# Performance work log

Hardware: AMD Instinct MI355X
Metric: run time of the kernel (lower is better)

The kernel has to match this reference:

```python
import jax, jax.numpy as jnp
import numpy as np

B, T, C, H, E, K = 4, 2048, 1024, 2048, 8, 2


def setup_inputs() -> dict:
    key = jax.random.key(0)
    ks = jax.random.split(key, 9)
    s = lambda k, shape, fan: jax.random.normal(k, shape, jnp.float32) / np.sqrt(fan)
    return {
        "x": jax.random.normal(ks[0], (B, T, C), jnp.float32),
        "gate_w": s(ks[1], (C, E), C),            # router gate (no bias)
        "sg_w": s(ks[2], (C, H), C),              # shared expert: gate proj
        "su_w": s(ks[3], (C, H), C),              # shared expert: up proj
        "sd_w": s(ks[4], (H, C), H),              # shared expert: down proj
        "eg_w": s(ks[5], (E, C, H), C),           # routed experts: gate proj
        "eu_w": s(ks[6], (E, C, H), C),           # routed experts: up proj
        "ed_w": s(ks[7], (E, H, C), H),           # routed experts: down proj
    }


def _swiglu(x, wg, wu, wd):
    # x: (B,T,C) -> (B,T,C)
    return jnp.einsum("bth,hc->btc", jax.nn.silu(jnp.einsum("btc,ch->bth", x, wg)) * jnp.einsum("btc,ch->bth", x, wu), wd)


def reference(x, gate_w, sg_w, su_w, sd_w, eg_w, eu_w, ed_w):
    # Router: top-k over expert logits, softmax over selected logits
    logits = jnp.einsum("btc,ce->bte", x, gate_w)            # (B,T,E)
    topk_logits, topk_idx = jax.lax.top_k(logits, K)         # (B,T,K)
    weights = jax.nn.softmax(topk_logits, axis=-1)           # (B,T,K)
    # Dense per-expert combine weight: w_e[b,t,e] = sum_k weights*(idx==e)
    onehot = jax.nn.one_hot(topk_idx, E, dtype=x.dtype)      # (B,T,K,E)
    dense_w = jnp.einsum("btk,btke->bte", weights, onehot)   # (B,T,E)

    shared_out = _swiglu(x, sg_w, su_w, sd_w)

    # Scan over experts (small fixed E), accumulating weighted expert outputs.
    dense_w_e = jnp.moveaxis(dense_w, -1, 0)                 # (E,B,T)

    def step(acc, params):
        wg, wu, wd, w = params
        return acc + w[..., None] * _swiglu(x, wg, wu, wd), None

    expert_out, _ = jax.lax.scan(step, jnp.zeros_like(x), (eg_w, eu_w, ed_w, dense_w_e))
    return shared_out + expert_out, logits
```

## Files before the change

### kernel.cpp

```cpp
#include <hip/hip_runtime.h>
#include <cstdint>
#include <cstddef>

#define NTOK 8192
#define CDIM 1024
#define HDIM 2048
#define NEXP 8
#define NSEG 9
#define MAXTILES 104

typedef __bf16 bf16;
typedef unsigned short u16;
typedef __attribute__((ext_vector_type(8))) __bf16 bf16x8;
typedef __attribute__((ext_vector_type(4))) float f32x4;

__device__ __forceinline__ u16 f2bf(float f) {
  union { u16 u; __bf16 b; } cv;
  cv.b = (__bf16)f;
  return cv.u;
}

__device__ __forceinline__ void gload_lds16(const bf16* g, bf16* l) {
  __builtin_amdgcn_global_load_lds(
      (const __attribute__((address_space(1))) unsigned int*)g,
      (__attribute__((address_space(3))) unsigned int*)l, 16, 0, 0);
}

__global__ __launch_bounds__(64) void init_kernel(int* __restrict__ counts,
                                                  int* __restrict__ fill) {
  if (threadIdx.x < NEXP) {
    counts[threadIdx.x] = 0;
    fill[threadIdx.x] = 0;
  }
}

__global__ __launch_bounds__(256) void zero_out_kernel(float* __restrict__ out) {
  size_t i = ((size_t)blockIdx.x * 256 + threadIdx.x) * 8;
  float4 z = {0.f, 0.f, 0.f, 0.f};
  *(float4*)(out + i) = z;
  *(float4*)(out + i + 4) = z;
}

__global__ __launch_bounds__(256) void cast_x_kernel(
    const float* __restrict__ src, bf16* __restrict__ dst) {
  size_t i = ((size_t)blockIdx.x * 256 + threadIdx.x) * 8;
  float4 a = *(const float4*)(src + i);
  float4 b = *(const float4*)(src + i + 4);
  bf16x8 p;
  p[0] = (bf16)a.x; p[1] = (bf16)a.y; p[2] = (bf16)a.z; p[3] = (bf16)a.w;
  p[4] = (bf16)b.x; p[5] = (bf16)b.y; p[6] = (bf16)b.z; p[7] = (bf16)b.w;
  *(bf16x8*)(dst + i) = p;
}

__global__ __launch_bounds__(256) void router2_kernel(
    const float* __restrict__ x, const float* __restrict__ gw,
    float* __restrict__ logits_out, int* __restrict__ tk_e,
    float* __restrict__ tk_w, int* __restrict__ counts) {
  int wv = threadIdx.x >> 6, l = threadIdx.x & 63;
  int t = blockIdx.x * 4 + wv;
  const float* xr = x + (size_t)t * CDIM;
  float acc[NEXP];
#pragma unroll
  for (int e = 0; e < NEXP; ++e) acc[e] = 0.f;
  for (int c = l; c < CDIM; c += 64) {
    float xv = xr[c];
    const float* g = gw + (size_t)c * NEXP;
    float4 g0 = *(const float4*)(g);
    float4 g1 = *(const float4*)(g + 4);
    acc[0] += xv * g0.x; acc[1] += xv * g0.y; acc[2] += xv * g0.z; acc[3] += xv * g0.w;
    acc[4] += xv * g1.x; acc[5] += xv * g1.y; acc[6] += xv * g1.z; acc[7] += xv * g1.w;
  }
#pragma unroll
  for (int off = 32; off > 0; off >>= 1) {
#pragma unroll
    for (int e = 0; e < NEXP; ++e) acc[e] += __shfl_xor(acc[e], off, 64);
  }
  int e0 = 0; float l0 = acc[0];
#pragma unroll
  for (int e = 1; e < NEXP; ++e) { if (acc[e] > l0) { l0 = acc[e]; e0 = e; } }
  int e1 = -1; float l1 = -3.4e38f;
#pragma unroll
  for (int e = 0; e < NEXP; ++e) { if (e != e0 && acc[e] > l1) { l1 = acc[e]; e1 = e; } }
  float ex = expf(l1 - l0);
  float w0 = 1.f / (1.f + ex), w1 = ex / (1.f + ex);
  if (l < NEXP) logits_out[(size_t)t * NEXP + l] = acc[l];
  if (l == 0) {
    tk_e[2 * t] = e0; tk_e[2 * t + 1] = e1;
    tk_w[2 * t] = w0; tk_w[2 * t + 1] = w1;
    atomicAdd(&counts[e0], 1);
    atomicAdd(&counts[e1], 1);
  }
}

__global__ __launch_bounds__(256) void offsets_kernel(
    const int* __restrict__ counts, int* __restrict__ offs_g,
    int* __restrict__ tile_seg, int* __restrict__ list_tok,
    float* __restrict__ w_row) {
  __shared__ int off[NSEG], pad[NSEG], cnt[NSEG], ntot;
  int tid = threadIdx.x;
  if (tid == 0) {
    int tot = 0;
    for (int e = 0; e < NSEG; ++e) {
      int c = (e < NEXP) ? counts[e] : NTOK;
      cnt[e] = c; off[e] = tot;
      int p = (c + 255) & ~255;
      pad[e] = p; tot += p;
    }
    ntot = tot;
  }
  __syncthreads();
  if (tid < NSEG) offs_g[tid] = off[tid];
  for (int gt = tid; gt < MAXTILES; gt += 256) {
    int row = gt * 256, seg = -1;
    if (row < ntot) {
      for (int e = 0; e < NSEG; ++e)
        if (row >= off[e] && row < off[e] + pad[e]) { seg = e; break; }
    }
    tile_seg[gt] = seg;
  }
  for (int e = 0; e < NSEG; ++e)
    for (int i = off[e] + cnt[e] + tid; i < off[e] + pad[e]; i += 256) {
      list_tok[i] = 0;
      w_row[i] = 0.f;
    }
}

__global__ __launch_bounds__(256) void scatter_kernel(
    const int* __restrict__ tk_e, const float* __restrict__ tk_w,
    const int* __restrict__ offs, int* __restrict__ fill,
    int* __restrict__ list_tok, float* __restrict__ w_row) {
  int t = blockIdx.x * 256 + threadIdx.x;
  int e0 = tk_e[2 * t], e1 = tk_e[2 * t + 1];
  float w0 = tk_w[2 * t], w1 = tk_w[2 * t + 1];
  int p0 = atomicAdd(&fill[e0], 1);
  int i0 = offs[e0] + p0;
  list_tok[i0] = t; w_row[i0] = w0;
  int p1 = atomicAdd(&fill[e1], 1);
  int i1 = offs[e1] + p1;
  list_tok[i1] = t; w_row[i1] = w1;
  int rsh = offs[NEXP] + t;
  list_tok[rsh] = t; w_row[rsh] = 1.f;
}

__device__ __forceinline__ void transpose_body(const float* __restrict__ src,
                                               u16* __restrict__ dst, int R, int C) {
  __shared__ u16 tile[64][65];
  int r0 = blockIdx.y * 64, c0 = blockIdx.x * 64;
  int tr = threadIdx.x >> 2;
  int tc = (threadIdx.x & 3) * 16;
  const float* s = src + (size_t)(r0 + tr) * C + c0 + tc;
  float4 f[4];
#pragma unroll
  for (int q = 0; q < 4; ++q) f[q] = *(const float4*)(s + q * 4);
#pragma unroll
  for (int q = 0; q < 4; ++q) {
    tile[tr][tc + q * 4 + 0] = f2bf(f[q].x);
    tile[tr][tc + q * 4 + 1] = f2bf(f[q].y);
    tile[tr][tc + q * 4 + 2] = f2bf(f[q].z);
    tile[tr][tc + q * 4 + 3] = f2bf(f[q].w);
  }
  __syncthreads();
  union { uint4 v[2]; u16 e[16]; } u;
#pragma unroll
  for (int j = 0; j < 16; ++j) u.e[j] = tile[tc + j][tr];
  u16* d = dst + (size_t)(c0 + tr) * R + r0 + tc;
  *(uint4*)d = u.v[0];
  *(uint4*)(d + 8) = u.v[1];
}

__global__ __launch_bounds__(256) void transpose_cast_kernel(
    const float* __restrict__ src, u16* __restrict__ dst, int R, int C) {
  transpose_body(src, dst, R, C);
}

__global__ __launch_bounds__(256) void transpose_gu_kernel(
    const float* __restrict__ sg, const float* __restrict__ su,
    const float* __restrict__ eg, const float* __restrict__ eu,
    u16* __restrict__ wTg, u16* __restrict__ wTu) {
  const size_t slot = (size_t)HDIM * CDIM;
  int z = blockIdx.z;
  const float* src; u16* dst;
  if (z == 0)       { src = sg;                 dst = wTg + 8 * slot; }
  else if (z == 1)  { src = su;                 dst = wTu + 8 * slot; }
  else if (z < 10)  { src = eg + (z - 2) * slot;  dst = wTg + (z - 2) * slot; }
  else              { src = eu + (z - 10) * slot; dst = wTu + (z - 10) * slot; }
  transpose_body(src, dst, CDIM, HDIM);
}

__global__ __launch_bounds__(256) void transpose_d_kernel(
    const float* __restrict__ sd, const float* __restrict__ ed,
    u16* __restrict__ wTd) {
  const size_t slot = (size_t)HDIM * CDIM;
  int z = blockIdx.z;
  const float* src; u16* dst;
  if (z == 0) { src = sd;                 dst = wTd + 8 * slot; }
  else        { src = ed + (z - 1) * slot; dst = wTd + (z - 1) * slot; }
  transpose_body(src, dst, HDIM, CDIM);
}


__global__ __launch_bounds__(512, 2) void gemm_gu4(
    const bf16* __restrict__ xb, const bf16* __restrict__ wTg,
    const bf16* __restrict__ wTu, const int* __restrict__ tile_seg,
    const int* __restrict__ list_tok, bf16* __restrict__ act) {
  __shared__ __align__(16) bf16 sS[2][32768];
  __shared__ int tokLds[256];

  const int nwg = gridDim.x;
  const int bid = blockIdx.x;
  const int wid = (bid & 7) * (nwg >> 3) + (bid >> 3);
  const int tileIdx = wid % MAXTILES;
  const int colIdx = wid / MAXTILES;
  const int seg = tile_seg[tileIdx];
  if (seg < 0) return;

  const int tid = threadIdx.x, l = tid & 63, wv = tid >> 6;
  const int wr = wv >> 2, wn = wv & 3;
  const int n0 = colIdx * 128;
  const size_t rowbase = (size_t)tileIdx * 256;

  if (tid < 256) tokLds[tid] = list_tok[rowbase + tid];
  __syncthreads();

  const int row8 = tid >> 3;
  const int scol = (((tid & 7) ^ (row8 & 7)) << 3);
  const bf16* gA0 = xb + (size_t)tokLds[row8] * CDIM + scol;
  const bf16* gA1 = xb + (size_t)tokLds[128 + row8] * CDIM + scol;
  const bf16* gA2 = xb + (size_t)tokLds[64 + row8] * CDIM + scol;
  const bf16* gA3 = xb + (size_t)tokLds[192 + row8] * CDIM + scol;
  const size_t wslot = (size_t)seg * HDIM * CDIM;
  const bf16* gBg = wTg + wslot + (size_t)(n0 + row8) * CDIM + scol;
  const bf16* gBu = wTu + wslot + (size_t)(n0 + row8) * CDIM + scol;
  const int t8 = tid * 8;

  const int fr = l & 15, kq = l >> 4;
  const int cS0 = ((kq ^ (l & 7)) << 4);
  const int cS1 = (((4 | kq) ^ (l & 7)) << 4);
  const int aBase = (wr * 128 + fr) * 128;
  const int gBase = 32768 + (wn * 32 + fr) * 128;
  const int uBase = 49152 + (wn * 32 + fr) * 128;

  f32x4 accG[2][4][2], accU[2][4][2];
#pragma unroll
  for (int h = 0; h < 2; ++h)
#pragma unroll
    for (int i = 0; i < 4; ++i)
#pragma unroll
      for (int j = 0; j < 2; ++j) {
        accG[h][i][j] = (f32x4){0.f, 0.f, 0.f, 0.f};
        accU[h][i][j] = (f32x4){0.f, 0.f, 0.f, 0.f};
      }

  auto stC0 = [&](int b, int k0) { bf16* d = &sS[b][0];
    gload_lds16(gBg + k0, d + 16384 + t8);
    gload_lds16(gBg + 64 * CDIM + k0, d + 20480 + t8); };
  auto stC1 = [&](int b, int k0) { bf16* d = &sS[b][0];
    gload_lds16(gA0 + k0, d + t8);
    gload_lds16(gA1 + k0, d + 8192 + t8); };
  auto stC2 = [&](int b, int k0) { bf16* d = &sS[b][0];
    gload_lds16(gBu + k0, d + 24576 + t8);
    gload_lds16(gBu + 64 * CDIM + k0, d + 28672 + t8); };
  auto stC3 = [&](int b, int k0) { bf16* d = &sS[b][0];
    gload_lds16(gA2 + k0, d + 4096 + t8);
    gload_lds16(gA3 + k0, d + 12288 + t8); };

  constexpr int NKT = CDIM / 64;
  stC0(0, 0); stC1(0, 0); stC2(0, 0); stC3(0, 0);

  for (int kt = 0; kt < NKT; ++kt) {
    const int b = kt & 1, bn = b ^ 1;
    const int kn = (kt + 1) * 64;
    const bool more = (kt + 1 < NKT);
    const char* pS = (const char*)&sS[b][0];
    bf16x8 af[4][2], bg[2][2], bu[2][2];

    asm volatile("s_waitcnt vmcnt(4)" ::: "memory");
    __builtin_amdgcn_s_barrier();
#pragma unroll
    for (int i = 0; i < 4; ++i) {
      af[i][0] = *(const bf16x8*)(pS + aBase + i * 2048 + cS0);
      af[i][1] = *(const bf16x8*)(pS + aBase + i * 2048 + cS1);
    }
#pragma unroll
    for (int j = 0; j < 2; ++j) {
      bg[j][0] = *(const bf16x8*)(pS + gBase + j * 2048 + cS0);
      bg[j][1] = *(const bf16x8*)(pS + gBase + j * 2048 + cS1);
    }
    if (more) stC0(bn, kn);
    asm volatile("s_waitcnt lgkmcnt(0)" ::: "memory");
    __builtin_amdgcn_sched_barrier(0);
    __builtin_amdgcn_s_setprio(1);
#pragma unroll
    for (int i = 0; i < 4; ++i)
#pragma unroll
      for (int j = 0; j < 2; ++j) {
        accG[0][i][j] = __builtin_amdgcn_mfma_f32_16x16x32_bf16(af[i][0], bg[j][0], accG[0][i][j], 0, 0, 0);
        accG[0][i][j] = __builtin_amdgcn_mfma_f32_16x16x32_bf16(af[i][1], bg[j][1], accG[0][i][j], 0, 0, 0);
      }
    __builtin_amdgcn_s_setprio(0);

    if (more) asm volatile("s_waitcnt vmcnt(4)" ::: "memory");
    else      asm volatile("s_waitcnt vmcnt(2)" ::: "memory");
    __builtin_amdgcn_s_barrier();
#pragma unroll
    for (int j = 0; j < 2; ++j) {
      bu[j][0] = *(const bf16x8*)(pS + uBase + j * 2048 + cS0);
      bu[j][1] = *(const bf16x8*)(pS + uBase + j * 2048 + cS1);
    }
    if (more) stC1(bn, kn);
    asm volatile("s_waitcnt lgkmcnt(0)" ::: "memory");
    __builtin_amdgcn_sched_barrier(0);
    __builtin_amdgcn_s_setprio(1);
#pragma unroll
    for (int i = 0; i < 4; ++i)
#pragma unroll
      for (int j = 0; j < 2; ++j) {
        accU[0][i][j] = __builtin_amdgcn_mfma_f32_16x16x32_bf16(af[i][0], bu[j][0], accU[0][i][j], 0, 0, 0);
        accU[0][i][j] = __builtin_amdgcn_mfma_f32_16x16x32_bf16(af[i][1], bu[j][1], accU[0][i][j], 0, 0, 0);
      }
    __builtin_amdgcn_s_setprio(0);

    if (more) asm volatile("s_waitcnt vmcnt(4)" ::: "memory");
    else      asm volatile("s_waitcnt vmcnt(0)" ::: "memory");
    __builtin_amdgcn_s_barrier();
#pragma unroll
    for (int i = 0; i < 4; ++i) {
      af[i][0] = *(const bf16x8*)(pS + aBase + 8192 + i * 2048 + cS0);
      af[i][1] = *(const bf16x8*)(pS + aBase + 8192 + i * 2048 + cS1);
    }
    if (more) stC2(bn, kn);
    asm volatile("s_waitcnt lgkmcnt(0)" ::: "memory");
    __builtin_amdgcn_sched_barrier(0);
    __builtin_amdgcn_s_setprio(1);
#pragma unroll
    for (int i = 0; i < 4; ++i)
#pragma unroll
      for (int j = 0; j < 2; ++j) {
        accG[1][i][j] = __builtin_amdgcn_mfma_f32_16x16x32_bf16(af[i][0], bg[j][0], accG[1][i][j], 0, 0, 0);
        accG[1][i][j] = __builtin_amdgcn_mfma_f32_16x16x32_bf16(af[i][1], bg[j][1], accG[1][i][j], 0, 0, 0);
      }
    __builtin_amdgcn_s_setprio(0);

    __builtin_amdgcn_s_barrier();
    if (more) stC3(bn, kn);
    __builtin_amdgcn_s_setprio(1);
#pragma unroll
    for (int i = 0; i < 4; ++i)
#pragma unroll
      for (int j = 0; j < 2; ++j) {
        accU[1][i][j] = __builtin_amdgcn_mfma_f32_16x16x32_bf16(af[i][0], bu[j][0], accU[1][i][j], 0, 0, 0);
        accU[1][i][j] = __builtin_amdgcn_mfma_f32_16x16x32_bf16(af[i][1], bu[j][1], accU[1][i][j], 0, 0, 0);
      }
    __builtin_amdgcn_s_setprio(0);
  }

  const int cn = n0 + wn * 32 + fr;
  const int rb = wr * 128 + kq * 4;
#pragma unroll
  for (int h = 0; h < 2; ++h)
#pragma unroll
    for (int i = 0; i < 4; ++i)
#pragma unroll
      for (int r = 0; r < 4; ++r) {
        const size_t row = rowbase + rb + h * 64 + i * 16 + r;
#pragma unroll
        for (int j = 0; j < 2; ++j) {
          float g = accG[h][i][j][r], uu = accU[h][i][j][r];
          float s = g / (1.f + expf(-g));
          act[row * HDIM + cn + j * 16] = (bf16)(s * uu);
        }
      }
}

__global__ __launch_bounds__(512, 2) void gemm_down4(
    const bf16* __restrict__ act, const bf16* __restrict__ wTd,
    const int* __restrict__ tile_seg, const int* __restrict__ list_tok,
    const float* __restrict__ w_row, float* __restrict__ out) {
  __shared__ __align__(16) bf16 sS[2][24576];
  __shared__ int tokLds[256];
  __shared__ float wLds[256];

  const int nwg = gridDim.x;
  const int bid = blockIdx.x;
  const int wid = (bid & 7) * (nwg >> 3) + (bid >> 3);
  const int tileIdx = wid % MAXTILES;
  const int colIdx = wid / MAXTILES;
  const int seg = tile_seg[tileIdx];
  if (seg < 0) return;

  const int tid = threadIdx.x, l = tid & 63, wv = tid >> 6;
  const int wr = wv >> 2, wn = wv & 3;
  const int n0 = colIdx * 128;
  const size_t rowbase = (size_t)tileIdx * 256;

  if (tid < 256) tokLds[tid] = list_tok[rowbase + tid];
  else           wLds[tid - 256] = w_row[rowbase + tid - 256];
  __syncthreads();

  const int row8 = tid >> 3;
  const int scol = (((tid & 7) ^ (row8 & 7)) << 3);
  const bf16* gA0 = act + (rowbase + row8) * HDIM + scol;
  const bf16* gA1 = act + (rowbase + 128 + row8) * HDIM + scol;
  const bf16* gA2 = act + (rowbase + 64 + row8) * HDIM + scol;
  const bf16* gA3 = act + (rowbase + 192 + row8) * HDIM + scol;
  const bf16* gB  = wTd + (size_t)seg * CDIM * HDIM + (size_t)(n0 + row8) * HDIM + scol;
  const int t8 = tid * 8;

  const int fr = l & 15, kq = l >> 4;
  const int cS0 = ((kq ^ (l & 7)) << 4);
  const int cS1 = (((4 | kq) ^ (l & 7)) << 4);
  const int aBase = (wr * 128 + fr) * 128;
  const int bBase = 32768 + (wn * 32 + fr) * 128;

  f32x4 acc[2][4][2];
#pragma unroll
  for (int h = 0; h < 2; ++h)
#pragma unroll
    for (int i = 0; i < 4; ++i)
#pragma unroll
      for (int j = 0; j < 2; ++j) acc[h][i][j] = (f32x4){0.f, 0.f, 0.f, 0.f};

  auto stC0 = [&](int b, int k0) { bf16* d = &sS[b][0];
    gload_lds16(gB + k0, d + 16384 + t8);
    gload_lds16(gB + 64 * HDIM + k0, d + 20480 + t8); };
  auto stC1 = [&](int b, int k0) { bf16* d = &sS[b][0];
    gload_lds16(gA0 + k0, d + t8);
    gload_lds16(gA1 + k0, d + 8192 + t8); };
  auto stC2 = [&](int b, int k0) { bf16* d = &sS[b][0];
    gload_lds16(gA2 + k0, d + 4096 + t8);
    gload_lds16(gA3 + k0, d + 12288 + t8); };

  constexpr int NKT = HDIM / 64;
  stC0(0, 0); stC1(0, 0); stC2(0, 0);

  for (int kt = 0; kt < NKT; ++kt) {
    const int b = kt & 1, bn = b ^ 1;
    const int kn = (kt + 1) * 64;
    const bool more = (kt + 1 < NKT);
    const char* pS = (const char*)&sS[b][0];
    bf16x8 af[4][2], bf[2][2];

    asm volatile("s_waitcnt vmcnt(2)" ::: "memory");
    __builtin_amdgcn_s_barrier();
#pragma unroll
    for (int i = 0; i < 4; ++i) {
      af[i][0] = *(const bf16x8*)(pS + aBase + i * 2048 + cS0);
      af[i][1] = *(const bf16x8*)(pS + aBase + i * 2048 + cS1);
    }
#pragma unroll
    for (int j = 0; j < 2; ++j) {
      bf[j][0] = *(const bf16x8*)(pS + bBase + j * 2048 + cS0);
      bf[j][1] = *(const bf16x8*)(pS + bBase + j * 2048 + cS1);
    }
    if (more) { stC0(bn, kn); stC1(bn, kn); }
    asm volatile("s_waitcnt lgkmcnt(0)" ::: "memory");
    __builtin_amdgcn_sched_barrier(0);
    __builtin_amdgcn_s_setprio(1);
#pragma unroll
    for (int i = 0; i < 4; ++i)
#pragma unroll
      for (int j = 0; j < 2; ++j) {
        acc[0][i][j] = __builtin_amdgcn_mfma_f32_16x16x32_bf16(af[i][0], bf[j][0], acc[0][i][j], 0, 0, 0);
        acc[0][i][j] = __builtin_amdgcn_mfma_f32_16x16x32_bf16(af[i][1], bf[j][1], acc[0][i][j], 0, 0, 0);
      }
    __builtin_amdgcn_s_setprio(0);

    if (more) asm volatile("s_waitcnt vmcnt(4)" ::: "memory");
    else      asm volatile("s_waitcnt vmcnt(0)" ::: "memory");
    __builtin_amdgcn_s_barrier();
#pragma unroll
    for (int i = 0; i < 4; ++i) {
      af[i][0] = *(const bf16x8*)(pS + aBase + 8192 + i * 2048 + cS0);
      af[i][1] = *(const bf16x8*)(pS + aBase + 8192 + i * 2048 + cS1);
    }
    if (more) stC2(bn, kn);
    asm volatile("s_waitcnt lgkmcnt(0)" ::: "memory");
    __builtin_amdgcn_sched_barrier(0);
    __builtin_amdgcn_s_setprio(1);
#pragma unroll
    for (int i = 0; i < 4; ++i)
#pragma unroll
      for (int j = 0; j < 2; ++j) {
        acc[1][i][j] = __builtin_amdgcn_mfma_f32_16x16x32_bf16(af[i][0], bf[j][0], acc[1][i][j], 0, 0, 0);
        acc[1][i][j] = __builtin_amdgcn_mfma_f32_16x16x32_bf16(af[i][1], bf[j][1], acc[1][i][j], 0, 0, 0);
      }
    __builtin_amdgcn_s_setprio(0);
  }

  const int cn = n0 + wn * 32 + fr;
  const int rb = wr * 128 + kq * 4;
#pragma unroll
  for (int h = 0; h < 2; ++h)
#pragma unroll
    for (int i = 0; i < 4; ++i)
#pragma unroll
      for (int r = 0; r < 4; ++r) {
        const int lrow = rb + h * 64 + i * 16 + r;
        const float w = wLds[lrow];
        if (w != 0.f) {
          const int tok = tokLds[lrow];
          float* op = out + (size_t)tok * CDIM + cn;
#pragma unroll
          for (int j = 0; j < 2; ++j)
            atomicAdd(op + j * 16, w * acc[h][i][j][r]);
        }
      }
}

__global__ __launch_bounds__(256) void router_kernel(
    const float* __restrict__ x, const float* __restrict__ gw,
    float* __restrict__ dense_w, float* __restrict__ logits_out) {
  int wv = threadIdx.x >> 6, l = threadIdx.x & 63;
  int t = blockIdx.x * 4 + wv;
  const float* xr = x + (size_t)t * CDIM;
  float acc[NEXP];
#pragma unroll
  for (int e = 0; e < NEXP; ++e) acc[e] = 0.f;
  for (int c = l; c < CDIM; c += 64) {
    float xv = xr[c];
    const float* g = gw + (size_t)c * NEXP;
    float4 g0 = *(const float4*)(g);
    float4 g1 = *(const float4*)(g + 4);
    acc[0] += xv * g0.x; acc[1] += xv * g0.y; acc[2] += xv * g0.z; acc[3] += xv * g0.w;
    acc[4] += xv * g1.x; acc[5] += xv * g1.y; acc[6] += xv * g1.z; acc[7] += xv * g1.w;
  }
#pragma unroll
  for (int off = 32; off > 0; off >>= 1) {
#pragma unroll
    for (int e = 0; e < NEXP; ++e) acc[e] += __shfl_xor(acc[e], off, 64);
  }
  int e0 = 0; float l0 = acc[0];
#pragma unroll
  for (int e = 1; e < NEXP; ++e) { if (acc[e] > l0) { l0 = acc[e]; e0 = e; } }
  int e1 = -1; float l1 = -3.4e38f;
#pragma unroll
  for (int e = 0; e < NEXP; ++e) { if (e != e0 && acc[e] > l1) { l1 = acc[e]; e1 = e; } }
  float ex = expf(l1 - l0);
  float w0 = 1.f / (1.f + ex), w1 = ex / (1.f + ex);
  if (l < NEXP) {
    dense_w[(size_t)t * NEXP + l] = (l == e0) ? w0 : ((l == e1) ? w1 : 0.f);
    logits_out[(size_t)t * NEXP + l] = acc[l];
  }
}

template <int MODE>
__global__ __launch_bounds__(256) void gemm_bt(
    const bf16* __restrict__ A, const bf16* __restrict__ Bt,
    int K, int N,
    bf16* __restrict__ Dbf, const bf16* __restrict__ Gin,
    float* __restrict__ outAcc, const float* __restrict__ denseW, int expertId) {
  __shared__ __align__(16) bf16 sA[128 * 32];
  __shared__ __align__(16) bf16 sB[128 * 32];
  const int tid = threadIdx.x;
  const int l = tid & 63, wv = tid >> 6;
  const int wr = wv >> 1, wc = wv & 1;
  const int m0 = blockIdx.y * 128, n0 = blockIdx.x * 128;
  f32x4 acc[4][4];
#pragma unroll
  for (int i = 0; i < 4; ++i)
#pragma unroll
    for (int j = 0; j < 4; ++j) acc[i][j] = (f32x4){0.f, 0.f, 0.f, 0.f};
  const int srow = wv * 16 + (l >> 2);
  const int scol = (l & 3) * 8;
  const bf16* gA = A + (size_t)(m0 + srow) * K + scol;
  const bf16* gB = Bt + (size_t)(n0 + srow) * K + scol;
  bf16* lA = sA + srow * 32 + scol;
  bf16* lB = sB + srow * 32 + scol;
  const int fr = l & 15, fk = (l >> 4) * 8;
  const bf16* rA = sA + (size_t)(wr * 64 + fr) * 32 + fk;
  const bf16* rB = sB + (size_t)(wc * 64 + fr) * 32 + fk;
  for (int k0 = 0; k0 < K; k0 += 32) {
    __syncthreads();
    gload_lds16(gA, lA);
    gload_lds16(gA + (size_t)64 * K, lA + 64 * 32);
    gload_lds16(gB, lB);
    gload_lds16(gB + (size_t)64 * K, lB + 64 * 32);
    gA += 32; gB += 32;
    __syncthreads();
    bf16x8 af[4], bfr[4];
#pragma unroll
    for (int i = 0; i < 4; ++i) af[i] = *(const bf16x8*)(rA + i * 16 * 32);
#pragma unroll
    for (int j = 0; j < 4; ++j) bfr[j] = *(const bf16x8*)(rB + j * 16 * 32);
#pragma unroll
    for (int i = 0; i < 4; ++i)
#pragma unroll
      for (int j = 0; j < 4; ++j)
        acc[i][j] = __builtin_amdgcn_mfma_f32_16x16x32_bf16(af[i], bfr[j], acc[i][j], 0, 0, 0);
  }
  const int cn = n0 + wc * 64 + (l & 15);
  const int rb = m0 + wr * 64 + (l >> 4) * 4;
#pragma unroll
  for (int i = 0; i < 4; ++i)
#pragma unroll
    for (int r = 0; r < 4; ++r) {
      const int m = rb + i * 16 + r;
#pragma unroll
      for (int j = 0; j < 4; ++j) {
        const int n = cn + j * 16;
        float v = acc[i][j][r];
        if (MODE == 0) {
          Dbf[(size_t)m * N + n] = (bf16)v;
        } else if (MODE == 1) {
          float g = (float)Gin[(size_t)m * N + n];
          float s = g / (1.f + expf(-g));
          Dbf[(size_t)m * N + n] = (bf16)(s * v);
        } else if (MODE == 2) {
          outAcc[(size_t)m * N + n] = v;
        } else {
          float w = denseW[(size_t)m * NEXP + expertId];
          outAcc[(size_t)m * N + n] += w * v;
        }
      }
    }
}

extern "C" void kernel_launch(void* const* d_in, const int* in_sizes, int n_in,
                              void* d_out, int out_size, void* d_ws, size_t ws_size,
                              hipStream_t stream) {
  const float* x    = (const float*)d_in[0];
  const float* gate = (const float*)d_in[1];
  const float* sg   = (const float*)d_in[2];
  const float* su   = (const float*)d_in[3];
  const float* sd   = (const float*)d_in[4];
  const float* eg   = (const float*)d_in[5];
  const float* eu   = (const float*)d_in[6];
  const float* ed   = (const float*)d_in[7];
  float* out    = (float*)d_out;
  float* logits = out + (size_t)NTOK * CDIM;

  const size_t MB = 1u << 20;
  const size_t full_need = 226 * MB;

  if (ws_size >= full_need) {
    char* ws = (char*)d_ws;
    bf16*  xb   = (bf16*)(ws);
    bf16*  wTg  = (bf16*)(ws + 16 * MB);
    bf16*  wTu  = (bf16*)(ws + 52 * MB);
    bf16*  act  = (bf16*)(ws + 88 * MB);
    bf16*  wTd  = (bf16*)(ws + 16 * MB);
    char*  sm   = ws + 224 * MB;
    int*   list_tok = (int*)(sm);
    int*   tk_e     = (int*)(sm + 256 * 1024);
    float* tk_w     = (float*)(sm + 320 * 1024);
    int*   tile_seg = (int*)(sm + 384 * 1024);
    int*   counts   = (int*)(sm + 388 * 1024);
    int*   fill     = (int*)(sm + 389 * 1024);
    int*   offs     = (int*)(sm + 390 * 1024);
    float* w_row    = (float*)(sm + 400 * 1024);

    init_kernel<<<1, 64, 0, stream>>>(counts, fill);
    zero_out_kernel<<<NTOK * CDIM / (256 * 8), 256, 0, stream>>>(out);
    cast_x_kernel<<<NTOK * CDIM / (256 * 8), 256, 0, stream>>>(x, xb);
    router2_kernel<<<NTOK / 4, 256, 0, stream>>>(x, gate, logits, tk_e, tk_w, counts);
    offsets_kernel<<<1, 256, 0, stream>>>(counts, offs, tile_seg, list_tok, w_row);
    scatter_kernel<<<NTOK / 256, 256, 0, stream>>>(tk_e, tk_w, offs, fill, list_tok, w_row);

    dim3 tgu(HDIM / 64, CDIM / 64, 18);
    transpose_gu_kernel<<<tgu, 256, 0, stream>>>(sg, su, eg, eu, (u16*)wTg, (u16*)wTu);

    gemm_gu4<<<(HDIM / 128) * MAXTILES, 512, 0, stream>>>(xb, wTg, wTu, tile_seg, list_tok, act);

    dim3 tdd(CDIM / 64, HDIM / 64, 9);
    transpose_d_kernel<<<tdd, 256, 0, stream>>>(sd, ed, (u16*)wTd);

    gemm_down4<<<(CDIM / 128) * MAXTILES, 512, 0, stream>>>(act, wTd, tile_seg, list_tok, w_row, out);
    return;
  }

  char* ws = (char*)d_ws;
  bf16*  xb   = (bf16*)(ws);
  bf16*  wTgf = (bf16*)(ws + 16 * MB);
  bf16*  wTuf = (bf16*)(ws + 20 * MB);
  bf16*  wTdf = (bf16*)(ws + 24 * MB);
  bf16*  gbuf = (bf16*)(ws + 28 * MB);
  float* dw   = (float*)(ws + 60 * MB);
  if (ws_size < 60 * MB + (size_t)NTOK * NEXP * sizeof(float)) return;

  cast_x_kernel<<<NTOK * CDIM / (256 * 8), 256, 0, stream>>>(x, xb);
  router_kernel<<<NTOK / 4, 256, 0, stream>>>(x, gate, dw, logits);

  dim3 tg1(HDIM / 64, CDIM / 64);
  dim3 tg2(CDIM / 64, HDIM / 64);
  dim3 g1(HDIM / 128, NTOK / 128);
  dim3 g2(CDIM / 128, NTOK / 128);

  transpose_cast_kernel<<<tg1, 256, 0, stream>>>(sg, (u16*)wTgf, CDIM, HDIM);
  transpose_cast_kernel<<<tg1, 256, 0, stream>>>(su, (u16*)wTuf, CDIM, HDIM);
  transpose_cast_kernel<<<tg2, 256, 0, stream>>>(sd, (u16*)wTdf, HDIM, CDIM);
  gemm_bt<0><<<g1, 256, 0, stream>>>(xb, wTgf, CDIM, HDIM, gbuf, nullptr, nullptr, nullptr, 0);
  gemm_bt<1><<<g1, 256, 0, stream>>>(xb, wTuf, CDIM, HDIM, gbuf, gbuf, nullptr, nullptr, 0);
  gemm_bt<2><<<g2, 256, 0, stream>>>(gbuf, wTdf, HDIM, CDIM, nullptr, nullptr, out, nullptr, 0);

  for (int e = 0; e < NEXP; ++e) {
    const float* egp = eg + (size_t)e * CDIM * HDIM;
    const float* eup = eu + (size_t)e * CDIM * HDIM;
    const float* edp = ed + (size_t)e * HDIM * CDIM;
    transpose_cast_kernel<<<tg1, 256, 0, stream>>>(egp, (u16*)wTgf, CDIM, HDIM);
    transpose_cast_kernel<<<tg1, 256, 0, stream>>>(eup, (u16*)wTuf, CDIM, HDIM);
    transpose_cast_kernel<<<tg2, 256, 0, stream>>>(edp, (u16*)wTdf, HDIM, CDIM);
    gemm_bt<0><<<g1, 256, 0, stream>>>(xb, wTgf, CDIM, HDIM, gbuf, nullptr, nullptr, nullptr, 0);
    gemm_bt<1><<<g1, 256, 0, stream>>>(xb, wTuf, CDIM, HDIM, gbuf, gbuf, nullptr, nullptr, 0);
    gemm_bt<3><<<g2, 256, 0, stream>>>(gbuf, wTdf, HDIM, CDIM, nullptr, nullptr, out, dw, e);
  }
}
```

Baseline: 969.1 us.

## Replace atomic scatter-add in down GEMM with bf16 buffer plus gather combine

The down-projection GEMM now writes its per-row results as bf16 into a dense buffer instead of doing weighted float atomicAdds into the output. A new combine kernel uses an inverse index map to gather each token's shared and two expert rows, weight them and write the output once, which also removes the output zeroing kernel and the w_row array. The transpose-cast body is also rewritten to pack two bf16 rows into 32-bit LDS words for wider shared-memory access. The trade is an extra kernel and buffer round trip, plus bf16 rounding of the intermediate expert outputs.

```diff
diff --git a/kernel.cpp b/kernel.cpp
--- a/kernel.cpp
+++ b/kernel.cpp
@@ -32,13 +32,6 @@
     counts[threadIdx.x] = 0;
     fill[threadIdx.x] = 0;
   }
-}
-
-__global__ __launch_bounds__(256) void zero_out_kernel(float* __restrict__ out) {
-  size_t i = ((size_t)blockIdx.x * 256 + threadIdx.x) * 8;
-  float4 z = {0.f, 0.f, 0.f, 0.f};
-  *(float4*)(out + i) = z;
-  *(float4*)(out + i + 4) = z;
 }
 
 __global__ __launch_bounds__(256) void cast_x_kernel(
@@ -94,8 +87,7 @@
 
 __global__ __launch_bounds__(256) void offsets_kernel(
     const int* __restrict__ counts, int* __restrict__ offs_g,
-    int* __restrict__ tile_seg, int* __restrict__ list_tok,
-    float* __restrict__ w_row) {
+    int* __restrict__ tile_seg, int* __restrict__ list_tok) {
   __shared__ int off[NSEG], pad[NSEG], cnt[NSEG], ntot;
   int tid = threadIdx.x;
   if (tid == 0) {
@@ -119,51 +111,56 @@
     tile_seg[gt] = seg;
   }
   for (int e = 0; e < NSEG; ++e)
-    for (int i = off[e] + cnt[e] + tid; i < off[e] + pad[e]; i += 256) {
+    for (int i = off[e] + cnt[e] + tid; i < off[e] + pad[e]; i += 256)
       list_tok[i] = 0;
-      w_row[i] = 0.f;
-    }
 }
 
 __global__ __launch_bounds__(256) void scatter_kernel(
-    const int* __restrict__ tk_e, const float* __restrict__ tk_w,
-    const int* __restrict__ offs, int* __restrict__ fill,
-    int* __restrict__ list_tok, float* __restrict__ w_row) {
+    const int* __restrict__ tk_e, const int* __restrict__ offs,
+    int* __restrict__ fill, int* __restrict__ list_tok,
+    int* __restrict__ inv) {
   int t = blockIdx.x * 256 + threadIdx.x;
   int e0 = tk_e[2 * t], e1 = tk_e[2 * t + 1];
-  float w0 = tk_w[2 * t], w1 = tk_w[2 * t + 1];
   int p0 = atomicAdd(&fill[e0], 1);
   int i0 = offs[e0] + p0;
-  list_tok[i0] = t; w_row[i0] = w0;
+  list_tok[i0] = t; inv[2 * t] = i0;
   int p1 = atomicAdd(&fill[e1], 1);
   int i1 = offs[e1] + p1;
-  list_tok[i1] = t; w_row[i1] = w1;
-  int rsh = offs[NEXP] + t;
-  list_tok[rsh] = t; w_row[rsh] = 1.f;
+  list_tok[i1] = t; inv[2 * t + 1] = i1;
+  list_tok[offs[NEXP] + t] = t;
 }
 
 __device__ __forceinline__ void transpose_body(const float* __restrict__ src,
                                                u16* __restrict__ dst, int R, int C) {
-  __shared__ u16 tile[64][65];
-  int r0 = blockIdx.y * 64, c0 = blockIdx.x * 64;
-  int tr = threadIdx.x >> 2;
-  int tc = (threadIdx.x & 3) * 16;
-  const float* s = src + (size_t)(r0 + tr) * C + c0 + tc;
-  float4 f[4];
-#pragma unroll
-  for (int q = 0; q < 4; ++q) f[q] = *(const float4*)(s + q * 4);
-#pragma unroll
-  for (int q = 0; q < 4; ++q) {
-    tile[tr][tc + q * 4 + 0] = f2bf(f[q].x);
-    tile[tr][tc + q * 4 + 1] = f2bf(f[q].y);
-    tile[tr][tc + q * 4 + 2] = f2bf(f[q].z);
-    tile[tr][tc + q * 4 + 3] = f2bf(f[q].w);
-  }
+  __shared__ uint32_t t32[64 * 33];
+  const int tid = threadIdx.x;
+  const int r0 = blockIdx.y * 64, c0 = blockIdx.x * 64;
+  const int rp = tid >> 3;
+  const int cg = tid & 7;
+  const float* s0 = src + (size_t)(r0 + 2 * rp) * C + c0 + 8 * cg;
+  const float* s1 = s0 + C;
+  float4 a0 = *(const float4*)(s0);
+  float4 a1 = *(const float4*)(s0 + 4);
+  float4 b0 = *(const float4*)(s1);
+  float4 b1 = *(const float4*)(s1 + 4);
+  uint32_t p[8];
+  p[0] = f2bf(a0.x) | ((uint32_t)f2bf(b0.x) << 16);
+  p[1] = f2bf(a0.y) | ((uint32_t)f2bf(b0.y) << 16);
+  p[2] = f2bf(a0.z) | ((uint32_t)f2bf(b0.z) << 16);
+  p[3] = f2bf(a0.w) | ((uint32_t)f2bf(b0.w) << 16);
+  p[4] = f2bf(a1.x) | ((uint32_t)f2bf(b1.x) << 16);
+  p[5] = f2bf(a1.y) | ((uint32_t)f2bf(b1.y) << 16);
+  p[6] = f2bf(a1.z) | ((uint32_t)f2bf(b1.z) << 16);
+  p[7] = f2bf(a1.w) | ((uint32_t)f2bf(b1.w) << 16);
+#pragma unroll
+  for (int c = 0; c < 8; ++c) t32[(8 * cg + c) * 33 + rp] = p[c];
   __syncthreads();
-  union { uint4 v[2]; u16 e[16]; } u;
-#pragma unroll
-  for (int j = 0; j < 16; ++j) u.e[j] = tile[tc + j][tr];
-  u16* d = dst + (size_t)(c0 + tr) * R + r0 + tc;
+  const int oc = tid >> 2, og = tid & 3;
+  const uint32_t* rb = &t32[oc * 33 + 8 * og];
+  union { uint32_t w[8]; uint4 v[2]; } u;
+#pragma unroll
+  for (int k = 0; k < 8; ++k) u.w[k] = rb[k];
+  u16* d = dst + (size_t)(c0 + oc) * R + r0 + 16 * og;
   *(uint4*)d = u.v[0];
   *(uint4*)(d + 8) = u.v[1];
 }
@@ -374,11 +371,8 @@
 
 __global__ __launch_bounds__(512, 2) void gemm_down4(
     const bf16* __restrict__ act, const bf16* __restrict__ wTd,
-    const int* __restrict__ tile_seg, const int* __restrict__ list_tok,
-    const float* __restrict__ w_row, float* __restrict__ out) {
+    const int* __restrict__ tile_seg, bf16* __restrict__ dbuf) {
   __shared__ __align__(16) bf16 sS[2][24576];
-  __shared__ int tokLds[256];
-  __shared__ float wLds[256];
 
   const int nwg = gridDim.x;
   const int bid = blockIdx.x;
@@ -392,10 +386,6 @@
   const int wr = wv >> 2, wn = wv & 3;
   const int n0 = colIdx * 128;
   const size_t rowbase = (size_t)tileIdx * 256;
-
-  if (tid < 256) tokLds[tid] = list_tok[rowbase + tid];
-  else           wLds[tid - 256] = w_row[rowbase + tid - 256];
-  __syncthreads();
 
   const int row8 = tid >> 3;
   const int scol = (((tid & 7) ^ (row8 & 7)) << 3);
@@ -495,16 +485,29 @@
     for (int i = 0; i < 4; ++i)
 #pragma unroll
       for (int r = 0; r < 4; ++r) {
-        const int lrow = rb + h * 64 + i * 16 + r;
-        const float w = wLds[lrow];
-        if (w != 0.f) {
-          const int tok = tokLds[lrow];
-          float* op = out + (size_t)tok * CDIM + cn;
-#pragma unroll
-          for (int j = 0; j < 2; ++j)
-            atomicAdd(op + j * 16, w * acc[h][i][j][r]);
-        }
-      }
+        const size_t row = rowbase + rb + h * 64 + i * 16 + r;
+#pragma unroll
+        for (int j = 0; j < 2; ++j)
+          dbuf[row * CDIM + cn + j * 16] = (bf16)acc[h][i][j][r];
+      }
+}
+
+__global__ __launch_bounds__(128) void combine_kernel(
+    const bf16* __restrict__ dbuf, const int* __restrict__ offs,
+    const int* __restrict__ inv, const float* __restrict__ tk_w,
+    float* __restrict__ out) {
+  const int t = blockIdx.x;
+  const int c = threadIdx.x * 8;
+  const int rsh = offs[NEXP] + t;
+  const int i0 = inv[2 * t], i1 = inv[2 * t + 1];
+  const float w0 = tk_w[2 * t], w1 = tk_w[2 * t + 1];
+  bf16x8 a = *(const bf16x8*)(dbuf + (size_t)rsh * CDIM + c);
+  bf16x8 b = *(const bf16x8*)(dbuf + (size_t)i0 * CDIM + c);
+  bf16x8 d = *(const bf16x8*)(dbuf + (size_t)i1 * CDIM + c);
+  float* op = out + (size_t)t * CDIM + c;
+#pragma unroll
+  for (int j = 0; j < 8; ++j)
+    op[j] = (float)a[j] + w0 * (float)b[j] + w1 * (float)d[j];
 }
 
 __global__ __launch_bounds__(256) void router_kernel(
@@ -638,23 +641,23 @@
     bf16*  wTg  = (bf16*)(ws + 16 * MB);
     bf16*  wTu  = (bf16*)(ws + 52 * MB);
     bf16*  act  = (bf16*)(ws + 88 * MB);
-    bf16*  wTd  = (bf16*)(ws + 16 * MB);
-    char*  sm   = ws + 224 * MB;
+    bf16*  wTd  = (bf16*)(ws);
+    bf16*  dbuf = (bf16*)(ws + 36 * MB);
+    char*  sm   = ws + 200 * MB;
     int*   list_tok = (int*)(sm);
+    int*   inv      = (int*)(sm + 128 * 1024);
     int*   tk_e     = (int*)(sm + 256 * 1024);
     float* tk_w     = (float*)(sm + 320 * 1024);
     int*   tile_seg = (int*)(sm + 384 * 1024);
     int*   counts   = (int*)(sm + 388 * 1024);
     int*   fill     = (int*)(sm + 389 * 1024);
     int*   offs     = (int*)(sm + 390 * 1024);
-    float* w_row    = (float*)(sm + 400 * 1024);
 
     init_kernel<<<1, 64, 0, stream>>>(counts, fill);
-    zero_out_kernel<<<NTOK * CDIM / (256 * 8), 256, 0, stream>>>(out);
     cast_x_kernel<<<NTOK * CDIM / (256 * 8), 256, 0, stream>>>(x, xb);
     router2_kernel<<<NTOK / 4, 256, 0, stream>>>(x, gate, logits, tk_e, tk_w, counts);
-    offsets_kernel<<<1, 256, 0, stream>>>(counts, offs, tile_seg, list_tok, w_row);
-    scatter_kernel<<<NTOK / 256, 256, 0, stream>>>(tk_e, tk_w, offs, fill, list_tok, w_row);
+    offsets_kernel<<<1, 256, 0, stream>>>(counts, offs, tile_seg, list_tok);
+    scatter_kernel<<<NTOK / 256, 256, 0, stream>>>(tk_e, offs, fill, list_tok, inv);
 
     dim3 tgu(HDIM / 64, CDIM / 64, 18);
     transpose_gu_kernel<<<tgu, 256, 0, stream>>>(sg, su, eg, eu, (u16*)wTg, (u16*)wTu);
@@ -664,7 +667,8 @@
     dim3 tdd(CDIM / 64, HDIM / 64, 9);
     transpose_d_kernel<<<tdd, 256, 0, stream>>>(sd, ed, (u16*)wTd);
 
-    gemm_down4<<<(CDIM / 128) * MAXTILES, 512, 0, stream>>>(act, wTd, tile_seg, list_tok, w_row, out);
+    gemm_down4<<<(CDIM / 128) * MAXTILES, 512, 0, stream>>>(act, wTd, tile_seg, dbuf);
+    combine_kernel<<<NTOK, 128, 0, stream>>>(dbuf, offs, inv, tk_w, out);
     return;
   }
 
```

New measurement: 917.8 us. 5.3% less time.
